# Kernel optimization log

Measured on AMD Instinct MI355X. Metric: run time of the kernel, lower is better.

## Reference

```python
import jax, jax.numpy as jnp
import numpy as np
from jax import lax

V, D_IN, H, B, T = 80, 8, 256, 4096, 80
W_SCALE = 1.0 / np.sqrt(H)  # matches torch nn.LSTM uniform init scale


def setup_inputs() -> dict:
    key = jax.random.key(0)
    ks = jax.random.split(key, 8)
    inp = {
        "x": jax.random.randint(ks[0], (B, T), 0, V),
        "h0": jnp.zeros((2, B, H), jnp.float32),
        "c0": jnp.zeros((2, B, H), jnp.float32),
        "emb": jax.random.normal(ks[1], (V, D_IN), jnp.float32),
        "W_ih0": jax.random.normal(ks[2], (4 * H, D_IN), jnp.float32) * W_SCALE,
        "W_hh0": jax.random.normal(ks[3], (4 * H, H), jnp.float32) * W_SCALE,
        "W_ih1": jax.random.normal(ks[4], (4 * H, H), jnp.float32) * W_SCALE,
        "W_hh1": jax.random.normal(ks[5], (4 * H, H), jnp.float32) * W_SCALE,
        "fc_W": jax.random.normal(ks[6], (V, H), jnp.float32) * W_SCALE,
        "fc_b": jnp.zeros((V,), jnp.float32),
    }
    return inp


def _lstm_layer(xs, h0, c0, W_ih, W_hh):
    # xs: [T, B, d_in]; precompute input contribution for all timesteps at once
    x_gates = jnp.einsum("tbd,gd->tbg", xs, W_ih)  # [T, B, 4H]

    def step(carry, xg):
        h, c = carry
        gates = xg + h @ W_hh.T  # [B, 4H], torch gate order i,f,g,o
        i, f, g, o = jnp.split(gates, 4, axis=-1)
        c = jax.nn.sigmoid(f) * c + jax.nn.sigmoid(i) * jnp.tanh(g)
        h = jax.nn.sigmoid(o) * jnp.tanh(c)
        return (h, c), h

    (hT, cT), hs = lax.scan(step, (h0, c0), x_gates)
    return hs, hT, cT  # hs: [T, B, H]


def reference(x, h0, c0, emb, W_ih0, W_hh0, W_ih1, W_hh1, fc_W, fc_b):
    xe = emb[x]                     # [B, T, D_IN] embedding lookup
    xs = jnp.swapaxes(xe, 0, 1)     # [T, B, D_IN] time-major for scan
    h1s, h1T, c1T = _lstm_layer(xs, h0[0], c0[0], W_ih0, W_hh0)
    h2s, h2T, c2T = _lstm_layer(h1s, h0[1], c0[1], W_ih1, W_hh1)
    logits = h2s[-1] @ fc_W.T + fc_b            # fc on last timestep: [B, V]
    h_n = jnp.stack([h1T, h2T])                  # [2, B, H]
    c_n = jnp.stack([c1T, c2T])
    return logits, h_n, c_n
```

## Files before the change

kernel.cpp:

```cpp
#include <hip/hip_runtime.h>
#include <hip/hip_bf16.h>
#include <stdint.h>

typedef __bf16 bf16x8 __attribute__((ext_vector_type(8)));
typedef float  f32x4  __attribute__((ext_vector_type(4)));

#define MFMA16(a, b, c) __builtin_amdgcn_mfma_f32_16x16x32_bf16((a), (b), (c), 0, 0, 0)

namespace {
constexpr int T_   = 80;
constexpr int B_   = 4096;
constexpr int H_   = 256;
constexpr int HP_  = 264;
constexpr int V_   = 80;
constexpr int RF   = 16;
constexpr int RC   = 32;
constexpr int NH   = 128;
constexpr int NTILE = 128;
constexpr int OUT_HN = B_ * V_;
constexpr int OUT_CN = OUT_HN + 2 * B_ * H_;

constexpr size_t WB_WHH0 = 0;
constexpr size_t WB_WIH1 = (size_t)1 << 20;
constexpr size_t WB_WHH1 = (size_t)2 << 20;
constexpr size_t WB_WIH0 = (size_t)3 << 20;
constexpr int WS_PLANE = 794624;
constexpr size_t WSB_XCHG  = 3178496;
constexpr size_t XCHG_U32  = (size_t)RC * NH;
constexpr size_t WSB_FLAGS = WSB_XCHG + (size_t)2 * 2 * NTILE * 2 * XCHG_U32 * 4;
constexpr int    CTRL_U32  = 512 + 256 + 8;
constexpr size_t WSB_TOTAL = WSB_FLAGS + (size_t)CTRL_U32 * 4;
}

__device__ __forceinline__ float sigm_(float x) { return 1.0f / (1.0f + __expf(-x)); }
__device__ __forceinline__ float tanh_(float x) {
  x = fminf(fmaxf(x, -15.f), 15.f);
  float e = __expf(2.f * x);
  return (e - 1.f) / (e + 1.f);
}

__device__ __forceinline__ void split_(float w, __hip_bfloat16* hi, __hip_bfloat16* lo) {
  __hip_bfloat16 h = __float2bfloat16(w);
  *hi = h;
  *lo = __float2bfloat16(w - __bfloat162float(h));
}

__device__ __forceinline__ uint32_t pack2_(__hip_bfloat16 hi, __hip_bfloat16 lo) {
  return (uint32_t)__builtin_bit_cast(unsigned short, hi) |
         ((uint32_t)__builtin_bit_cast(unsigned short, lo) << 16);
}
__device__ __forceinline__ __hip_bfloat16 ubf_(unsigned short v) {
  return __builtin_bit_cast(__hip_bfloat16, v);
}

__device__ __forceinline__ void ldfrag_(const char* pp, bf16x8* h, bf16x8* l) {
  *h = *(const bf16x8*)pp;
  *l = *(const bf16x8*)(pp + 16);
}

__device__ __forceinline__ size_t addrK256_(int e) {
  int row = e >> 8, kk = e & 255;
  int g = row >> 8, cb = row & 255, t = cb >> 4, m = cb & 15;
  int k = kk >> 5, quad = (kk >> 3) & 3, j = kk & 7;
  return (size_t)(((t * 8 + k) * 4 + g)) * 2048 + (size_t)((quad * 16 + m) * 32 + j * 2);
}

__global__ __launch_bounds__(256) void cvt_pair(
    const float* __restrict__ Wih0f, const float* __restrict__ Whh0f,
    const float* __restrict__ Wih1f, const float* __restrict__ Whh1f,
    __hip_bfloat16* __restrict__ ws, int zero_flags)
{
  if (zero_flags && blockIdx.x < 4) {
    uint32_t* fl = (uint32_t*)((char*)ws + WSB_FLAGS);
    int idx = blockIdx.x * 256 + threadIdx.x;
    if (idx < CTRL_U32) fl[idx] = 0u;
  }
  int i = blockIdx.x * 256 + threadIdx.x;
  if (i >= WS_PLANE) return;
  char* wb = (char*)ws;
  float v; size_t off;
  if (i < 262144) {
    v = Whh0f[i];            off = WB_WHH0 + addrK256_(i);
  } else if (i < 524288) {
    int e = i - 262144;
    v = Wih1f[e];            off = WB_WIH1 + addrK256_(e);
  } else if (i < 786432) {
    int e = i - 524288;
    v = Whh1f[e];            off = WB_WHH1 + addrK256_(e);
  } else {
    int e = i - 786432;
    int row = e >> 3, j = e & 7;
    int g = row >> 8, cb = row & 255, t = cb >> 4, m = cb & 15;
    v = Wih0f[e];
    off = WB_WIH0 + (size_t)((t * 4 + g) * 512 + m * 32 + j * 2);
  }
  __hip_bfloat16 hi = __float2bfloat16(v);
  *(__hip_bfloat16*)(wb + off)      = hi;
  *(__hip_bfloat16*)(wb + off + 16) = __float2bfloat16(v - __bfloat162float(hi));
}

__device__ __forceinline__ f32x4 tri_(bf16x8 ahi, bf16x8 alo, bf16x8 bhi, bf16x8 blo, f32x4 acc) {
  acc = MFMA16(ahi, bhi, acc);
  acc = MFMA16(ahi, blo, acc);
  acc = MFMA16(alo, bhi, acc);
  return acc;
}

__global__ __attribute__((amdgpu_waves_per_eu(2, 2))) __launch_bounds__(512)
void lstm_coop(
    const int* __restrict__ x,
    const float* __restrict__ h0,
    const float* __restrict__ c0,
    const float* __restrict__ emb,
    const __hip_bfloat16* __restrict__ wsW,
    const float* __restrict__ fcW,
    const float* __restrict__ fcb,
    float* __restrict__ out)
{
  __shared__ __align__(16) __hip_bfloat16 h1s[2][2][RC][HP_];
  __shared__ __align__(16) __hip_bfloat16 h2s[2][RC][HP_];
  __shared__ __align__(16) __hip_bfloat16 embs[2][V_][8];
  __shared__ unsigned short toks[RC][T_];
  __shared__ int slot_s;

  const int tid  = threadIdx.x;
  const int lane = tid & 63;
  const int wv   = tid >> 6;
  const int m    = lane & 15;
  const int quad = lane >> 4;
  const int jw   = wv * 16;
  const int lane32 = lane << 5;

  uint32_t* xch   = (uint32_t*)((char*)wsW + WSB_XCHG);
  uint32_t* flags = (uint32_t*)((char*)wsW + WSB_FLAGS);
  uint32_t* owner = flags + 512;
  uint32_t* cnt   = flags + 768;

  if (tid == 0) {
    uint32_t xcd;
    asm volatile("s_getreg_b32 %0, hwreg(20, 0, 4)" : "=s"(xcd));
    xcd &= 7u;
    uint32_t rank = atomicAdd(&cnt[xcd], 1u) & 31u;
    int p = (int)((xcd * 32u + rank) & 255u);
    while (atomicCAS(&owner[p], 0u, 1u) != 0u) p = (p + 1) & 255;
    slot_s = p;
  }
  __syncthreads();
  const int slot = slot_s;
  const int vx   = slot >> 5;
  const int rank = slot & 31;
  const int half = vx >> 2;
  const int tile = (vx & 3) * 32 + rank;
  const int r0   = tile * RC;
  const int oh   = half ^ 1;
  const int colb = half * NH + jw + m;
  const int tcol = half * 8 + wv;

  const char* wb    = (const char*)wsW;
  const char* pWhh0 = wb + WB_WHH0;
  const char* pWih1 = wb + WB_WIH1;
  const char* pWhh1 = wb + WB_WHH1;
  const char* pWih0 = wb + WB_WIH0;

  uint32_t* fl_own  = flags + half * NTILE + tile;
  uint32_t* fl_prt  = flags + oh   * NTILE + tile;
  uint32_t* fl_own1 = flags + 2 * NTILE + half * NTILE + tile;
  uint32_t* fl_prt1 = flags + 2 * NTILE + oh   * NTILE + tile;

  uint32_t* xo0 = xch + (((size_t)(0 * 2 + half) * NTILE + tile) * 2) * XCHG_U32;
  const uint32_t* xi0 = xch + (((size_t)(0 * 2 + oh) * NTILE + tile) * 2) * XCHG_U32;
  uint32_t* xo1 = xch + (((size_t)(1 * 2 + half) * NTILE + tile) * 2) * XCHG_U32;
  const uint32_t* xi1 = xch + (((size_t)(1 * 2 + oh) * NTILE + tile) * 2) * XCHG_U32;

  if (tid < V_) {
#pragma unroll
    for (int j = 0; j < 8; ++j)
      split_(emb[tid * 8 + j], &embs[0][tid][j], &embs[1][tid][j]);
  }
  for (int i = tid; i < RC * T_; i += 512) {
    int r = i / T_, tt = i - r * T_;
    int tok = x[(r0 + r) * T_ + tt];
    toks[r][tt] = (unsigned short)(tok < 0 ? 0 : (tok >= V_ ? V_ - 1 : tok));
  }
  for (int i = tid; i < RC * H_; i += 512) {
    int r = i >> 8, cc = i & 255;
    split_(h0[(0 * B_ + r0 + r) * H_ + cc], &h1s[1][0][r][cc], &h1s[1][1][r][cc]);
    split_(h0[(1 * B_ + r0 + r) * H_ + cc], &h2s[0][r][cc],    &h2s[1][r][cc]);
  }
  f32x4 c1[2], c2[2];
#pragma unroll
  for (int mt = 0; mt < 2; ++mt)
#pragma unroll
    for (int r = 0; r < 4; ++r) {
      int row = r0 + mt * 16 + quad * 4 + r;
      c1[mt][r] = c0[(0 * B_ + row) * H_ + colb];
      c2[mt][r] = c0[(1 * B_ + row) * H_ + colb];
    }

  bf16x8 zb;
#pragma unroll
  for (int j = 0; j < 8; ++j) zb[j] = (__bf16)0.0f;
  const f32x4 zf = {0.f, 0.f, 0.f, 0.f};

  __syncthreads();

  for (int t = 0; t < T_; ++t) {
    const int p = t & 1, q = p ^ 1;

    f32x4 acc[2][4];
    bf16x8 B0h[2][4], B0l[2][4];
#pragma unroll
    for (int g = 0; g < 4; ++g)
      ldfrag_(pWhh0 + ((size_t)((tcol * 8 + 0) * 4 + g) << 11) + lane32,
              &B0h[0][g], &B0l[0][g]);
    {
      bf16x8 eh0 = zb, el0 = zb, eh1 = zb, el1 = zb;
      if (quad == 0) {
        int t0 = toks[m][t], t1 = toks[16 + m][t];
        eh0 = *(const bf16x8*)&embs[0][t0][0]; el0 = *(const bf16x8*)&embs[1][t0][0];
        eh1 = *(const bf16x8*)&embs[0][t1][0]; el1 = *(const bf16x8*)&embs[1][t1][0];
      }
#pragma unroll
      for (int g = 0; g < 4; ++g) {
        bf16x8 Bh, Bl;
        ldfrag_(pWih0 + (size_t)((tcol * 4 + g) * 512 + (m << 5)), &Bh, &Bl);
        acc[0][g] = tri_(eh0, el0, Bh, Bl, zf);
        acc[1][g] = tri_(eh1, el1, Bh, Bl, zf);
      }
    }
#pragma unroll
    for (int k = 0; k < 8; ++k) {
      const int kb = k & 1, kn = kb ^ 1;
      if (k < 7) {
#pragma unroll
        for (int g = 0; g < 4; ++g)
          ldfrag_(pWhh0 + ((size_t)((tcol * 8 + k + 1) * 4 + g) << 11) + lane32,
                  &B0h[kn][g], &B0l[kn][g]);
      }
      const int ko = k * 32 + quad * 8;
      bf16x8 Ah0 = *(const bf16x8*)&h1s[q][0][m][ko];
      bf16x8 Al0 = *(const bf16x8*)&h1s[q][1][m][ko];
      bf16x8 Ah1 = *(const bf16x8*)&h1s[q][0][16 + m][ko];
      bf16x8 Al1 = *(const bf16x8*)&h1s[q][1][16 + m][ko];
#pragma unroll
      for (int g = 0; g < 4; ++g) {
        acc[0][g] = tri_(Ah0, Al0, B0h[kb][g], B0l[kb][g], acc[0][g]);
        acc[1][g] = tri_(Ah1, Al1, B0h[kb][g], B0l[kb][g], acc[1][g]);
      }
    }

    bf16x8 W1h[2][4], W1l[2][4];
#pragma unroll
    for (int g = 0; g < 4; ++g)
      ldfrag_(pWhh1 + ((size_t)((tcol * 8 + 0) * 4 + g) << 11) + lane32,
              &W1h[0][g], &W1l[0][g]);

    {
      uint32_t* xo = xo0 + (size_t)p * XCHG_U32;
#pragma unroll
      for (int mt = 0; mt < 2; ++mt)
#pragma unroll
        for (int r = 0; r < 4; ++r) {
          float ig = sigm_(acc[mt][0][r]);
          float fg = sigm_(acc[mt][1][r]);
          float gg = tanh_(acc[mt][2][r]);
          float og = sigm_(acc[mt][3][r]);
          float cn = fg * c1[mt][r] + ig * gg;
          c1[mt][r] = cn;
          float hv = og * tanh_(cn);
          int rr = mt * 16 + quad * 4 + r;
          __hip_bfloat16 hi, lo;
          split_(hv, &hi, &lo);
          h1s[p][0][rr][colb] = hi;
          h1s[p][1][rr][colb] = lo;
          __hip_atomic_store(&xo[rr * NH + jw + m], pack2_(hi, lo),
                             __ATOMIC_RELAXED, __HIP_MEMORY_SCOPE_AGENT);
        }
    }
    __syncthreads();
    if (tid == 0) {
      __hip_atomic_store(fl_own, (uint32_t)(t + 1),
                         __ATOMIC_RELAXED, __HIP_MEMORY_SCOPE_AGENT);
      while (__hip_atomic_load(fl_prt1, __ATOMIC_RELAXED,
                               __HIP_MEMORY_SCOPE_AGENT) < (uint32_t)t)
        __builtin_amdgcn_s_sleep(2);
    }
    __syncthreads();
    if (t > 0) {
      const uint64_t* xj = (const uint64_t*)(xi1 + (size_t)q * XCHG_U32);
      for (int i = tid; i < RC * NH / 2; i += 512) {
        uint64_t u = __hip_atomic_load(&xj[i], __ATOMIC_RELAXED, __HIP_MEMORY_SCOPE_AGENT);
        int row = i >> 6, c2 = (i & 63) * 2;
        uint32_t w0 = (uint32_t)u, w1 = (uint32_t)(u >> 32);
        h2s[0][row][oh * NH + c2]     = ubf_((unsigned short)(w0 & 0xffffu));
        h2s[1][row][oh * NH + c2]     = ubf_((unsigned short)(w0 >> 16));
        h2s[0][row][oh * NH + c2 + 1] = ubf_((unsigned short)(w1 & 0xffffu));
        h2s[1][row][oh * NH + c2 + 1] = ubf_((unsigned short)(w1 >> 16));
      }
    }
    __syncthreads();

#pragma unroll
    for (int mt = 0; mt < 2; ++mt)
#pragma unroll
      for (int g = 0; g < 4; ++g) acc[mt][g] = zf;
#pragma unroll
    for (int k = 0; k < 8; ++k) {
      const int kb = k & 1, kn = kb ^ 1;
      if (k < 7) {
#pragma unroll
        for (int g = 0; g < 4; ++g)
          ldfrag_(pWhh1 + ((size_t)((tcol * 8 + k + 1) * 4 + g) << 11) + lane32,
                  &W1h[kn][g], &W1l[kn][g]);
      }
      const int ko = k * 32 + quad * 8;
      bf16x8 Ch0 = *(const bf16x8*)&h2s[0][m][ko];
      bf16x8 Cl0 = *(const bf16x8*)&h2s[1][m][ko];
      bf16x8 Ch1 = *(const bf16x8*)&h2s[0][16 + m][ko];
      bf16x8 Cl1 = *(const bf16x8*)&h2s[1][16 + m][ko];
#pragma unroll
      for (int g = 0; g < 4; ++g) {
        acc[0][g] = tri_(Ch0, Cl0, W1h[kb][g], W1l[kb][g], acc[0][g]);
        acc[1][g] = tri_(Ch1, Cl1, W1h[kb][g], W1l[kb][g], acc[1][g]);
      }
    }

    bf16x8 W2h[2][4], W2l[2][4];
#pragma unroll
    for (int g = 0; g < 4; ++g)
      ldfrag_(pWih1 + ((size_t)((tcol * 8 + 0) * 4 + g) << 11) + lane32,
              &W2h[0][g], &W2l[0][g]);

    if (tid == 0) {
      while (__hip_atomic_load(fl_prt, __ATOMIC_RELAXED,
                               __HIP_MEMORY_SCOPE_AGENT) < (uint32_t)(t + 1))
        __builtin_amdgcn_s_sleep(2);
    }
    __syncthreads();
    {
      const uint64_t* xi = (const uint64_t*)(xi0 + (size_t)p * XCHG_U32);
      for (int i = tid; i < RC * NH / 2; i += 512) {
        uint64_t u = __hip_atomic_load(&xi[i], __ATOMIC_RELAXED, __HIP_MEMORY_SCOPE_AGENT);
        int row = i >> 6, c2 = (i & 63) * 2;
        uint32_t w0 = (uint32_t)u, w1 = (uint32_t)(u >> 32);
        h1s[p][0][row][oh * NH + c2]     = ubf_((unsigned short)(w0 & 0xffffu));
        h1s[p][1][row][oh * NH + c2]     = ubf_((unsigned short)(w0 >> 16));
        h1s[p][0][row][oh * NH + c2 + 1] = ubf_((unsigned short)(w1 & 0xffffu));
        h1s[p][1][row][oh * NH + c2 + 1] = ubf_((unsigned short)(w1 >> 16));
      }
    }
    __syncthreads();

#pragma unroll
    for (int k = 0; k < 8; ++k) {
      const int kb = k & 1, kn = kb ^ 1;
      if (k < 7) {
#pragma unroll
        for (int g = 0; g < 4; ++g)
          ldfrag_(pWih1 + ((size_t)((tcol * 8 + k + 1) * 4 + g) << 11) + lane32,
                  &W2h[kn][g], &W2l[kn][g]);
      }
      const int ko = k * 32 + quad * 8;
      bf16x8 Ah0 = *(const bf16x8*)&h1s[p][0][m][ko];
      bf16x8 Al0 = *(const bf16x8*)&h1s[p][1][m][ko];
      bf16x8 Ah1 = *(const bf16x8*)&h1s[p][0][16 + m][ko];
      bf16x8 Al1 = *(const bf16x8*)&h1s[p][1][16 + m][ko];
#pragma unroll
      for (int g = 0; g < 4; ++g) {
        acc[0][g] = tri_(Ah0, Al0, W2h[kb][g], W2l[kb][g], acc[0][g]);
        acc[1][g] = tri_(Ah1, Al1, W2h[kb][g], W2l[kb][g], acc[1][g]);
      }
    }

    {
      uint32_t* xo = xo1 + (size_t)p * XCHG_U32;
#pragma unroll
      for (int mt = 0; mt < 2; ++mt)
#pragma unroll
        for (int r = 0; r < 4; ++r) {
          float ig = sigm_(acc[mt][0][r]);
          float fg = sigm_(acc[mt][1][r]);
          float gg = tanh_(acc[mt][2][r]);
          float og = sigm_(acc[mt][3][r]);
          float cn = fg * c2[mt][r] + ig * gg;
          c2[mt][r] = cn;
          float hv = og * tanh_(cn);
          int rr = mt * 16 + quad * 4 + r;
          __hip_bfloat16 hi, lo;
          split_(hv, &hi, &lo);
          h2s[0][rr][colb] = hi;
          h2s[1][rr][colb] = lo;
          __hip_atomic_store(&xo[rr * NH + jw + m], pack2_(hi, lo),
                             __ATOMIC_RELAXED, __HIP_MEMORY_SCOPE_AGENT);
        }
    }
    __syncthreads();
    if (tid == 0)
      __hip_atomic_store(fl_own1, (uint32_t)(t + 1),
                         __ATOMIC_RELAXED, __HIP_MEMORY_SCOPE_AGENT);
  }

  if (tid == 0) {
    while (__hip_atomic_load(fl_prt1, __ATOMIC_RELAXED,
                             __HIP_MEMORY_SCOPE_AGENT) < (uint32_t)T_)
      __builtin_amdgcn_s_sleep(2);
  }
  __syncthreads();
  {
    const uint64_t* xj = (const uint64_t*)(xi1 + (size_t)((T_ - 1) & 1) * XCHG_U32);
    for (int i = tid; i < RC * NH / 2; i += 512) {
      uint64_t u = __hip_atomic_load(&xj[i], __ATOMIC_RELAXED, __HIP_MEMORY_SCOPE_AGENT);
      int row = i >> 6, c2 = (i & 63) * 2;
      uint32_t w0 = (uint32_t)u, w1 = (uint32_t)(u >> 32);
      h2s[0][row][oh * NH + c2]     = ubf_((unsigned short)(w0 & 0xffffu));
      h2s[1][row][oh * NH + c2]     = ubf_((unsigned short)(w0 >> 16));
      h2s[0][row][oh * NH + c2 + 1] = ubf_((unsigned short)(w1 & 0xffffu));
      h2s[1][row][oh * NH + c2 + 1] = ubf_((unsigned short)(w1 >> 16));
    }
  }
  __syncthreads();

  const int pf = (T_ - 1) & 1;

  for (int i = tid; i < RC * NH; i += 512) {
    int r = i >> 7, c = i & (NH - 1), col = half * NH + c;
    out[OUT_HN + (0 * B_ + r0 + r) * H_ + col] =
        __bfloat162float(h1s[pf][0][r][col]) + __bfloat162float(h1s[pf][1][r][col]);
    out[OUT_HN + (1 * B_ + r0 + r) * H_ + col] =
        __bfloat162float(h2s[0][r][col]) + __bfloat162float(h2s[1][r][col]);
  }
#pragma unroll
  for (int mt = 0; mt < 2; ++mt)
#pragma unroll
    for (int r = 0; r < 4; ++r) {
      int row = r0 + mt * 16 + quad * 4 + r;
      out[OUT_CN + row * H_ + colb]           = c1[mt][r];
      out[OUT_CN + B_ * H_ + row * H_ + colb] = c2[mt][r];
    }
  for (int i = tid; i < RC * (V_ / 2); i += 512) {
    int r = i / (V_ / 2), v = half * (V_ / 2) + i % (V_ / 2);
    const float* wp = fcW + v * H_;
    float s = fcb[v];
#pragma unroll 8
    for (int k = 0; k < H_; ++k) {
      float hk = __bfloat162float(h2s[0][r][k]) + __bfloat162float(h2s[1][r][k]);
      s += hk * wp[k];
    }
    out[(r0 + r) * V_ + v] = s;
  }
}

template<bool USE_WS>
__device__ __forceinline__ void loadB_(const char* wtb, int grp, int lane,
                                       const float* wf, int off,
                                       bf16x8* bhi, bf16x8* blo) {
  if (USE_WS) {
    const char* pp = wtb + ((size_t)grp << 11) + (lane << 5);
    *bhi = *(const bf16x8*)pp;
    *blo = *(const bf16x8*)(pp + 16);
  } else {
    f32x4 a = *(const f32x4*)(wf + off);
    f32x4 b = *(const f32x4*)(wf + off + 4);
#pragma unroll
    for (int j = 0; j < 4; ++j) {
      float w = a[j]; __bf16 h = (__bf16)w;
      (*bhi)[j] = h; (*blo)[j] = (__bf16)(w - (float)h);
    }
#pragma unroll
    for (int j = 0; j < 4; ++j) {
      float w = b[j]; __bf16 h = (__bf16)w;
      (*bhi)[4 + j] = h; (*blo)[4 + j] = (__bf16)(w - (float)h);
    }
  }
}

template<bool USE_WS>
__global__ __launch_bounds__(512, 2) void lstm_fused(
    const int* __restrict__ x,
    const float* __restrict__ h0,
    const float* __restrict__ c0,
    const float* __restrict__ emb,
    const __hip_bfloat16* __restrict__ wsW,
    const float* __restrict__ Wih0f,
    const float* __restrict__ Whh0f,
    const float* __restrict__ Wih1f,
    const float* __restrict__ Whh1f,
    const float* __restrict__ fcW,
    const float* __restrict__ fcb,
    float* __restrict__ out)
{
  __shared__ __align__(16) __hip_bfloat16 h1s[2][2][RF][HP_];
  __shared__ __align__(16) __hip_bfloat16 h2s[2][RF][HP_];
  __shared__ __align__(16) __hip_bfloat16 embs[2][V_][8];
  __shared__ __align__(16) __hip_bfloat16 es[2][RF][8];

  const int tid  = threadIdx.x;
  const int lane = tid & 63;
  const int wv   = tid >> 6;
  const int m    = lane & 15;
  const int quad = lane >> 4;
  const int jw   = wv * 32;
  const int r0   = blockIdx.x * RF;
  const char* wb = (const char*)wsW;

  if (tid < V_) {
#pragma unroll
    for (int j = 0; j < 8; ++j)
      split_(emb[tid * 8 + j], &embs[0][tid][j], &embs[1][tid][j]);
  }
  for (int i = tid; i < RF * H_; i += 512) {
    int r = i >> 8, cc = i & 255;
    split_(h0[(0 * B_ + r0 + r) * H_ + cc], &h1s[1][0][r][cc], &h1s[1][1][r][cc]);
    split_(h0[(1 * B_ + r0 + r) * H_ + cc], &h2s[0][r][cc],    &h2s[1][r][cc]);
  }
  f32x4 c1[2], c2[2];
#pragma unroll
  for (int ct = 0; ct < 2; ++ct)
#pragma unroll
    for (int r = 0; r < 4; ++r) {
      int row = r0 + quad * 4 + r;
      int col = jw + ct * 16 + m;
      c1[ct][r] = c0[(0 * B_ + row) * H_ + col];
      c2[ct][r] = c0[(1 * B_ + row) * H_ + col];
    }

  bf16x8 zb;
#pragma unroll
  for (int j = 0; j < 8; ++j) zb[j] = (__bf16)0.0f;
  const f32x4 zf = {0.f, 0.f, 0.f, 0.f};

  __syncthreads();

  for (int t = 0; t < T_; ++t) {
    const int p = t & 1, q = p ^ 1;

    if (tid < RF) {
      int tok = x[(r0 + tid) * T_ + t];
      tok = tok < 0 ? 0 : (tok >= V_ ? V_ - 1 : tok);
      *(bf16x8*)&es[0][tid][0] = *(const bf16x8*)&embs[0][tok][0];
      *(bf16x8*)&es[1][tid][0] = *(const bf16x8*)&embs[1][tok][0];
    }
    __syncthreads();

    f32x4 acc[8];
    {
      bf16x8 eh = zb, el = zb;
      if (quad == 0) {
        eh = *(const bf16x8*)&es[0][m][0];
        el = *(const bf16x8*)&es[1][m][0];
      }
#pragma unroll
      for (int g = 0; g < 4; ++g)
#pragma unroll
        for (int ct = 0; ct < 2; ++ct) {
          bf16x8 Bh = zb, Bl = zb;
          if (quad == 0) {
            if (USE_WS) {
              const char* pp = wb + WB_WIH0 +
                               (size_t)(((wv * 2 + ct) * 4 + g) * 512 + (m << 5));
              Bh = *(const bf16x8*)pp;
              Bl = *(const bf16x8*)(pp + 16);
            } else {
              const int off = (g * 256 + jw + ct * 16 + m) * 8;
              loadB_<false>(nullptr, 0, 0, Wih0f, off, &Bh, &Bl);
            }
          }
          acc[g * 2 + ct] = tri_(eh, el, Bh, Bl, zf);
        }
    }
#pragma unroll
    for (int k = 0; k < 8; ++k) {
      const int ko = k * 32 + quad * 8;
      bf16x8 Ah = *(const bf16x8*)&h1s[q][0][m][ko];
      bf16x8 Al = *(const bf16x8*)&h1s[q][1][m][ko];
#pragma unroll
      for (int g = 0; g < 4; ++g)
#pragma unroll
        for (int ct = 0; ct < 2; ++ct) {
          bf16x8 Bh, Bl;
          const int grp = ((wv * 2 + ct) * 8 + k) * 4 + g;
          const int off = (g * 256 + jw + ct * 16 + m) * H_ + ko;
          loadB_<USE_WS>(wb + WB_WHH0, grp, lane, Whh0f, off, &Bh, &Bl);
          acc[g * 2 + ct] = tri_(Ah, Al, Bh, Bl, acc[g * 2 + ct]);
        }
    }
#pragma unroll
    for (int ct = 0; ct < 2; ++ct)
#pragma unroll
      for (int r = 0; r < 4; ++r) {
        float ig = sigm_(acc[0 + ct][r]);
        float fg = sigm_(acc[2 + ct][r]);
        float gg = tanh_(acc[4 + ct][r]);
        float og = sigm_(acc[6 + ct][r]);
        float cn = fg * c1[ct][r] + ig * gg;
        c1[ct][r] = cn;
        float hv = og * tanh_(cn);
        int rr = quad * 4 + r, col = jw + ct * 16 + m;
        split_(hv, &h1s[p][0][rr][col], &h1s[p][1][rr][col]);
      }
    __syncthreads();

#pragma unroll
    for (int nt = 0; nt < 8; ++nt) acc[nt] = zf;
#pragma unroll
    for (int k = 0; k < 8; ++k) {
      const int ko = k * 32 + quad * 8;
      bf16x8 Ah = *(const bf16x8*)&h1s[p][0][m][ko];
      bf16x8 Al = *(const bf16x8*)&h1s[p][1][m][ko];
      bf16x8 Ch = *(const bf16x8*)&h2s[0][m][ko];
      bf16x8 Cl = *(const bf16x8*)&h2s[1][m][ko];
#pragma unroll
      for (int g = 0; g < 4; ++g)
#pragma unroll
        for (int ct = 0; ct < 2; ++ct) {
          const int grp = ((wv * 2 + ct) * 8 + k) * 4 + g;
          const int off = (g * 256 + jw + ct * 16 + m) * H_ + ko;
          bf16x8 Bh, Bl;
          loadB_<USE_WS>(wb + WB_WIH1, grp, lane, Wih1f, off, &Bh, &Bl);
          acc[g * 2 + ct] = tri_(Ah, Al, Bh, Bl, acc[g * 2 + ct]);
          loadB_<USE_WS>(wb + WB_WHH1, grp, lane, Whh1f, off, &Bh, &Bl);
          acc[g * 2 + ct] = tri_(Ch, Cl, Bh, Bl, acc[g * 2 + ct]);
        }
    }
    __syncthreads();

#pragma unroll
    for (int ct = 0; ct < 2; ++ct)
#pragma unroll
      for (int r = 0; r < 4; ++r) {
        float ig = sigm_(acc[0 + ct][r]);
        float fg = sigm_(acc[2 + ct][r]);
        float gg = tanh_(acc[4 + ct][r]);
        float og = sigm_(acc[6 + ct][r]);
        float cn = fg * c2[ct][r] + ig * gg;
        c2[ct][r] = cn;
        float hv = og * tanh_(cn);
        int rr = quad * 4 + r, col = jw + ct * 16 + m;
        split_(hv, &h2s[0][rr][col], &h2s[1][rr][col]);
      }
  }
  __syncthreads();

  const int pf = (T_ - 1) & 1;

  for (int i = tid; i < RF * H_; i += 512) {
    int r = i >> 8, cc = i & 255;
    out[OUT_HN + (0 * B_ + r0 + r) * H_ + cc] =
        __bfloat162float(h1s[pf][0][r][cc]) + __bfloat162float(h1s[pf][1][r][cc]);
    out[OUT_HN + (1 * B_ + r0 + r) * H_ + cc] =
        __bfloat162float(h2s[0][r][cc]) + __bfloat162float(h2s[1][r][cc]);
  }
#pragma unroll
  for (int ct = 0; ct < 2; ++ct)
#pragma unroll
    for (int r = 0; r < 4; ++r) {
      int row = r0 + quad * 4 + r;
      int col = jw + ct * 16 + m;
      out[OUT_CN + row * H_ + col]           = c1[ct][r];
      out[OUT_CN + B_ * H_ + row * H_ + col] = c2[ct][r];
    }
  for (int i = tid; i < RF * V_; i += 512) {
    int r = i / V_, v = i - r * V_;
    const float* wp = fcW + v * H_;
    float s = fcb[v];
#pragma unroll 8
    for (int k = 0; k < H_; ++k) {
      float hk = __bfloat162float(h2s[0][r][k]) + __bfloat162float(h2s[1][r][k]);
      s += hk * wp[k];
    }
    out[(r0 + r) * V_ + v] = s;
  }
}

extern "C" void kernel_launch(void* const* d_in, const int* in_sizes, int n_in,
                              void* d_out, int out_size, void* d_ws, size_t ws_size,
                              hipStream_t stream) {
  (void)in_sizes; (void)n_in; (void)out_size;
  const int*   x    = (const int*)d_in[0];
  const float* h0   = (const float*)d_in[1];
  const float* c0   = (const float*)d_in[2];
  const float* emb  = (const float*)d_in[3];
  const float* Wih0 = (const float*)d_in[4];
  const float* Whh0 = (const float*)d_in[5];
  const float* Wih1 = (const float*)d_in[6];
  const float* Whh1 = (const float*)d_in[7];
  const float* fcW  = (const float*)d_in[8];
  const float* fcb  = (const float*)d_in[9];
  float* outp = (float*)d_out;

  __hip_bfloat16* wsW = (__hip_bfloat16*)d_ws;

  if (ws_size >= WSB_TOTAL) {
    cvt_pair<<<(WS_PLANE + 255) / 256, 256, 0, stream>>>(Wih0, Whh0, Wih1, Whh1, wsW, 1);
    void* args[] = { (void*)&x, (void*)&h0, (void*)&c0, (void*)&emb, (void*)&wsW,
                     (void*)&fcW, (void*)&fcb, (void*)&outp };
    hipLaunchCooperativeKernel(reinterpret_cast<void*>(lstm_coop),
                               dim3(256), dim3(512), args, 0, stream);
  } else if (ws_size >= WSB_XCHG) {
    cvt_pair<<<(WS_PLANE + 255) / 256, 256, 0, stream>>>(Wih0, Whh0, Wih1, Whh1, wsW, 0);
    lstm_fused<true><<<B_ / RF, 512, 0, stream>>>(
        x, h0, c0, emb, wsW, Wih0, Whh0, Wih1, Whh1, fcW, fcb, outp);
  } else {
    lstm_fused<false><<<B_ / RF, 512, 0, stream>>>(
        x, h0, c0, emb, wsW, Wih0, Whh0, Wih1, Whh1, fcW, fcb, outp);
  }
}
```

Before: 3.064 ms.

## Split each tile's rows across two wave groups with 1024-thread blocks

Doubles the cooperative kernel's block to 1024 threads. Each group of 8 waves now handles 16 of the 32 rows per tile instead of each wave computing both 16-row M-tiles. This halves per-wave MFMA work and accumulator registers per timestep, putting more waves on the serial recurrence. The cost is that both row groups load the same weight fragments, which doubles weight traffic from global/L2 per block, and block-wide barriers now span more waves.

```diff
diff --git a/kernel.cpp b/kernel.cpp
--- a/kernel.cpp
+++ b/kernel.cpp
@@ -106,7 +106,7 @@
   return acc;
 }
 
-__global__ __attribute__((amdgpu_waves_per_eu(2, 2))) __launch_bounds__(512)
+__global__ __launch_bounds__(1024, 4)
 void lstm_coop(
     const int* __restrict__ x,
     const float* __restrict__ h0,
@@ -128,7 +128,10 @@
   const int wv   = tid >> 6;
   const int m    = lane & 15;
   const int quad = lane >> 4;
-  const int jw   = wv * 16;
+  const int ct   = wv & 7;
+  const int rh   = wv >> 3;
+  const int rbase = rh * 16;
+  const int jw   = ct * 16;
   const int lane32 = lane << 5;
 
   uint32_t* xch   = (uint32_t*)((char*)wsW + WSB_XCHG);
@@ -154,7 +157,7 @@
   const int r0   = tile * RC;
   const int oh   = half ^ 1;
   const int colb = half * NH + jw + m;
-  const int tcol = half * 8 + wv;
+  const int tcol = half * 8 + ct;
 
   const char* wb    = (const char*)wsW;
   const char* pWhh0 = wb + WB_WHH0;
@@ -177,25 +180,23 @@
     for (int j = 0; j < 8; ++j)
       split_(emb[tid * 8 + j], &embs[0][tid][j], &embs[1][tid][j]);
   }
-  for (int i = tid; i < RC * T_; i += 512) {
+  for (int i = tid; i < RC * T_; i += 1024) {
     int r = i / T_, tt = i - r * T_;
     int tok = x[(r0 + r) * T_ + tt];
     toks[r][tt] = (unsigned short)(tok < 0 ? 0 : (tok >= V_ ? V_ - 1 : tok));
   }
-  for (int i = tid; i < RC * H_; i += 512) {
+  for (int i = tid; i < RC * H_; i += 1024) {
     int r = i >> 8, cc = i & 255;
     split_(h0[(0 * B_ + r0 + r) * H_ + cc], &h1s[1][0][r][cc], &h1s[1][1][r][cc]);
     split_(h0[(1 * B_ + r0 + r) * H_ + cc], &h2s[0][r][cc],    &h2s[1][r][cc]);
   }
-  f32x4 c1[2], c2[2];
-#pragma unroll
-  for (int mt = 0; mt < 2; ++mt)
-#pragma unroll
-    for (int r = 0; r < 4; ++r) {
-      int row = r0 + mt * 16 + quad * 4 + r;
-      c1[mt][r] = c0[(0 * B_ + row) * H_ + colb];
-      c2[mt][r] = c0[(1 * B_ + row) * H_ + colb];
-    }
+  f32x4 c1, c2;
+#pragma unroll
+  for (int r = 0; r < 4; ++r) {
+    int row = r0 + rbase + quad * 4 + r;
+    c1[r] = c0[(0 * B_ + row) * H_ + colb];
+    c2[r] = c0[(1 * B_ + row) * H_ + colb];
+  }
 
   bf16x8 zb;
 #pragma unroll
@@ -207,25 +208,24 @@
   for (int t = 0; t < T_; ++t) {
     const int p = t & 1, q = p ^ 1;
 
-    f32x4 acc[2][4];
+    f32x4 acc[4];
     bf16x8 B0h[2][4], B0l[2][4];
 #pragma unroll
     for (int g = 0; g < 4; ++g)
       ldfrag_(pWhh0 + ((size_t)((tcol * 8 + 0) * 4 + g) << 11) + lane32,
               &B0h[0][g], &B0l[0][g]);
     {
-      bf16x8 eh0 = zb, el0 = zb, eh1 = zb, el1 = zb;
+      bf16x8 eh = zb, el = zb;
       if (quad == 0) {
-        int t0 = toks[m][t], t1 = toks[16 + m][t];
-        eh0 = *(const bf16x8*)&embs[0][t0][0]; el0 = *(const bf16x8*)&embs[1][t0][0];
-        eh1 = *(const bf16x8*)&embs[0][t1][0]; el1 = *(const bf16x8*)&embs[1][t1][0];
+        int t0 = toks[rbase + m][t];
+        eh = *(const bf16x8*)&embs[0][t0][0];
+        el = *(const bf16x8*)&embs[1][t0][0];
       }
 #pragma unroll
       for (int g = 0; g < 4; ++g) {
         bf16x8 Bh, Bl;
         ldfrag_(pWih0 + (size_t)((tcol * 4 + g) * 512 + (m << 5)), &Bh, &Bl);
-        acc[0][g] = tri_(eh0, el0, Bh, Bl, zf);
-        acc[1][g] = tri_(eh1, el1, Bh, Bl, zf);
+        acc[g] = tri_(eh, el, Bh, Bl, zf);
       }
     }
 #pragma unroll
@@ -238,15 +238,11 @@
                   &B0h[kn][g], &B0l[kn][g]);
       }
       const int ko = k * 32 + quad * 8;
-      bf16x8 Ah0 = *(const bf16x8*)&h1s[q][0][m][ko];
-      bf16x8 Al0 = *(const bf16x8*)&h1s[q][1][m][ko];
-      bf16x8 Ah1 = *(const bf16x8*)&h1s[q][0][16 + m][ko];
-      bf16x8 Al1 = *(const bf16x8*)&h1s[q][1][16 + m][ko];
-#pragma unroll
-      for (int g = 0; g < 4; ++g) {
-        acc[0][g] = tri_(Ah0, Al0, B0h[kb][g], B0l[kb][g], acc[0][g]);
-        acc[1][g] = tri_(Ah1, Al1, B0h[kb][g], B0l[kb][g], acc[1][g]);
-      }
+      bf16x8 Ah = *(const bf16x8*)&h1s[q][0][rbase + m][ko];
+      bf16x8 Al = *(const bf16x8*)&h1s[q][1][rbase + m][ko];
+#pragma unroll
+      for (int g = 0; g < 4; ++g)
+        acc[g] = tri_(Ah, Al, B0h[kb][g], B0l[kb][g], acc[g]);
     }
 
     bf16x8 W1h[2][4], W1l[2][4];
@@ -258,24 +254,22 @@
     {
       uint32_t* xo = xo0 + (size_t)p * XCHG_U32;
 #pragma unroll
-      for (int mt = 0; mt < 2; ++mt)
-#pragma unroll
-        for (int r = 0; r < 4; ++r) {
-          float ig = sigm_(acc[mt][0][r]);
-          float fg = sigm_(acc[mt][1][r]);
-          float gg = tanh_(acc[mt][2][r]);
-          float og = sigm_(acc[mt][3][r]);
-          float cn = fg * c1[mt][r] + ig * gg;
-          c1[mt][r] = cn;
-          float hv = og * tanh_(cn);
-          int rr = mt * 16 + quad * 4 + r;
-          __hip_bfloat16 hi, lo;
-          split_(hv, &hi, &lo);
-          h1s[p][0][rr][colb] = hi;
-          h1s[p][1][rr][colb] = lo;
-          __hip_atomic_store(&xo[rr * NH + jw + m], pack2_(hi, lo),
-                             __ATOMIC_RELAXED, __HIP_MEMORY_SCOPE_AGENT);
-        }
+      for (int r = 0; r < 4; ++r) {
+        float ig = sigm_(acc[0][r]);
+        float fg = sigm_(acc[1][r]);
+        float gg = tanh_(acc[2][r]);
+        float og = sigm_(acc[3][r]);
+        float cn = fg * c1[r] + ig * gg;
+        c1[r] = cn;
+        float hv = og * tanh_(cn);
+        int rr = rbase + quad * 4 + r;
+        __hip_bfloat16 hi, lo;
+        split_(hv, &hi, &lo);
+        h1s[p][0][rr][colb] = hi;
+        h1s[p][1][rr][colb] = lo;
+        __hip_atomic_store(&xo[rr * NH + jw + m], pack2_(hi, lo),
+                           __ATOMIC_RELAXED, __HIP_MEMORY_SCOPE_AGENT);
+      }
     }
     __syncthreads();
     if (tid == 0) {
@@ -288,22 +282,20 @@
     __syncthreads();
     if (t > 0) {
       const uint64_t* xj = (const uint64_t*)(xi1 + (size_t)q * XCHG_U32);
-      for (int i = tid; i < RC * NH / 2; i += 512) {
+      for (int i = tid; i < RC * NH / 2; i += 1024) {
         uint64_t u = __hip_atomic_load(&xj[i], __ATOMIC_RELAXED, __HIP_MEMORY_SCOPE_AGENT);
-        int row = i >> 6, c2 = (i & 63) * 2;
+        int row = i >> 6, c2v = (i & 63) * 2;
         uint32_t w0 = (uint32_t)u, w1 = (uint32_t)(u >> 32);
-        h2s[0][row][oh * NH + c2]     = ubf_((unsigned short)(w0 & 0xffffu));
-        h2s[1][row][oh * NH + c2]     = ubf_((unsigned short)(w0 >> 16));
-        h2s[0][row][oh * NH + c2 + 1] = ubf_((unsigned short)(w1 & 0xffffu));
-        h2s[1][row][oh * NH + c2 + 1] = ubf_((unsigned short)(w1 >> 16));
-      }
-    }
-    __syncthreads();
-
-#pragma unroll
-    for (int mt = 0; mt < 2; ++mt)
-#pragma unroll
-      for (int g = 0; g < 4; ++g) acc[mt][g] = zf;
+        h2s[0][row][oh * NH + c2v]     = ubf_((unsigned short)(w0 & 0xffffu));
+        h2s[1][row][oh * NH + c2v]     = ubf_((unsigned short)(w0 >> 16));
+        h2s[0][row][oh * NH + c2v + 1] = ubf_((unsigned short)(w1 & 0xffffu));
+        h2s[1][row][oh * NH + c2v + 1] = ubf_((unsigned short)(w1 >> 16));
+      }
+    }
+    __syncthreads();
+
+#pragma unroll
+    for (int g = 0; g < 4; ++g) acc[g] = zf;
 #pragma unroll
     for (int k = 0; k < 8; ++k) {
       const int kb = k & 1, kn = kb ^ 1;
@@ -314,15 +306,11 @@
                   &W1h[kn][g], &W1l[kn][g]);
       }
       const int ko = k * 32 + quad * 8;
-      bf16x8 Ch0 = *(const bf16x8*)&h2s[0][m][ko];
-      bf16x8 Cl0 = *(const bf16x8*)&h2s[1][m][ko];
-      bf16x8 Ch1 = *(const bf16x8*)&h2s[0][16 + m][ko];
-      bf16x8 Cl1 = *(const bf16x8*)&h2s[1][16 + m][ko];
-#pragma unroll
-      for (int g = 0; g < 4; ++g) {
-        acc[0][g] = tri_(Ch0, Cl0, W1h[kb][g], W1l[kb][g], acc[0][g]);
-        acc[1][g] = tri_(Ch1, Cl1, W1h[kb][g], W1l[kb][g], acc[1][g]);
-      }
+      bf16x8 Ch = *(const bf16x8*)&h2s[0][rbase + m][ko];
+      bf16x8 Cl = *(const bf16x8*)&h2s[1][rbase + m][ko];
+#pragma unroll
+      for (int g = 0; g < 4; ++g)
+        acc[g] = tri_(Ch, Cl, W1h[kb][g], W1l[kb][g], acc[g]);
     }
 
     bf16x8 W2h[2][4], W2l[2][4];
@@ -339,14 +327,14 @@
     __syncthreads();
     {
       const uint64_t* xi = (const uint64_t*)(xi0 + (size_t)p * XCHG_U32);
-      for (int i = tid; i < RC * NH / 2; i += 512) {
+      for (int i = tid; i < RC * NH / 2; i += 1024) {
         uint64_t u = __hip_atomic_load(&xi[i], __ATOMIC_RELAXED, __HIP_MEMORY_SCOPE_AGENT);
-        int row = i >> 6, c2 = (i & 63) * 2;
+        int row = i >> 6, c2v = (i & 63) * 2;
         uint32_t w0 = (uint32_t)u, w1 = (uint32_t)(u >> 32);
-        h1s[p][0][row][oh * NH + c2]     = ubf_((unsigned short)(w0 & 0xffffu));
-        h1s[p][1][row][oh * NH + c2]     = ubf_((unsigned short)(w0 >> 16));
-        h1s[p][0][row][oh * NH + c2 + 1] = ubf_((unsigned short)(w1 & 0xffffu));
-        h1s[p][1][row][oh * NH + c2 + 1] = ubf_((unsigned short)(w1 >> 16));
+        h1s[p][0][row][oh * NH + c2v]     = ubf_((unsigned short)(w0 & 0xffffu));
+        h1s[p][1][row][oh * NH + c2v]     = ubf_((unsigned short)(w0 >> 16));
+        h1s[p][0][row][oh * NH + c2v + 1] = ubf_((unsigned short)(w1 & 0xffffu));
+        h1s[p][1][row][oh * NH + c2v + 1] = ubf_((unsigned short)(w1 >> 16));
       }
     }
     __syncthreads();
@@ -361,38 +349,32 @@
                   &W2h[kn][g], &W2l[kn][g]);
       }
       const int ko = k * 32 + quad * 8;
-      bf16x8 Ah0 = *(const bf16x8*)&h1s[p][0][m][ko];
-      bf16x8 Al0 = *(const bf16x8*)&h1s[p][1][m][ko];
-      bf16x8 Ah1 = *(const bf16x8*)&h1s[p][0][16 + m][ko];
-      bf16x8 Al1 = *(const bf16x8*)&h1s[p][1][16 + m][ko];
-#pragma unroll
-      for (int g = 0; g < 4; ++g) {
-        acc[0][g] = tri_(Ah0, Al0, W2h[kb][g], W2l[kb][g], acc[0][g]);
-        acc[1][g] = tri_(Ah1, Al1, W2h[kb][g], W2l[kb][g], acc[1][g]);
-      }
+      bf16x8 Ah = *(const bf16x8*)&h1s[p][0][rbase + m][ko];
+      bf16x8 Al = *(const bf16x8*)&h1s[p][1][rbase + m][ko];
+#pragma unroll
+      for (int g = 0; g < 4; ++g)
+        acc[g] = tri_(Ah, Al, W2h[kb][g], W2l[kb][g], acc[g]);
     }
 
     {
       uint32_t* xo = xo1 + (size_t)p * XCHG_U32;
 #pragma unroll
-      for (int mt = 0; mt < 2; ++mt)
-#pragma unroll
-        for (int r = 0; r < 4; ++r) {
-          float ig = sigm_(acc[mt][0][r]);
-          float fg = sigm_(acc[mt][1][r]);
-          float gg = tanh_(acc[mt][2][r]);
-          float og = sigm_(acc[mt][3][r]);
-          float cn = fg * c2[mt][r] + ig * gg;
-          c2[mt][r] = cn;
-          float hv = og * tanh_(cn);
-          int rr = mt * 16 + quad * 4 + r;
-          __hip_bfloat16 hi, lo;
-          split_(hv, &hi, &lo);
-          h2s[0][rr][colb] = hi;
-          h2s[1][rr][colb] = lo;
-          __hip_atomic_store(&xo[rr * NH + jw + m], pack2_(hi, lo),
-                             __ATOMIC_RELAXED, __HIP_MEMORY_SCOPE_AGENT);
-        }
+      for (int r = 0; r < 4; ++r) {
+        float ig = sigm_(acc[0][r]);
+        float fg = sigm_(acc[1][r]);
+        float gg = tanh_(acc[2][r]);
+        float og = sigm_(acc[3][r]);
+        float cn = fg * c2[r] + ig * gg;
+        c2[r] = cn;
+        float hv = og * tanh_(cn);
+        int rr = rbase + quad * 4 + r;
+        __hip_bfloat16 hi, lo;
+        split_(hv, &hi, &lo);
+        h2s[0][rr][colb] = hi;
+        h2s[1][rr][colb] = lo;
+        __hip_atomic_store(&xo[rr * NH + jw + m], pack2_(hi, lo),
+                           __ATOMIC_RELAXED, __HIP_MEMORY_SCOPE_AGENT);
+      }
     }
     __syncthreads();
     if (tid == 0)
@@ -408,21 +390,21 @@
   __syncthreads();
   {
     const uint64_t* xj = (const uint64_t*)(xi1 + (size_t)((T_ - 1) & 1) * XCHG_U32);
-    for (int i = tid; i < RC * NH / 2; i += 512) {
+    for (int i = tid; i < RC * NH / 2; i += 1024) {
       uint64_t u = __hip_atomic_load(&xj[i], __ATOMIC_RELAXED, __HIP_MEMORY_SCOPE_AGENT);
-      int row = i >> 6, c2 = (i & 63) * 2;
+      int row = i >> 6, c2v = (i & 63) * 2;
       uint32_t w0 = (uint32_t)u, w1 = (uint32_t)(u >> 32);
-      h2s[0][row][oh * NH + c2]     = ubf_((unsigned short)(w0 & 0xffffu));
-      h2s[1][row][oh * NH + c2]     = ubf_((unsigned short)(w0 >> 16));
-      h2s[0][row][oh * NH + c2 + 1] = ubf_((unsigned short)(w1 & 0xffffu));
-      h2s[1][row][oh * NH + c2 + 1] = ubf_((unsigned short)(w1 >> 16));
+      h2s[0][row][oh * NH + c2v]     = ubf_((unsigned short)(w0 & 0xffffu));
+      h2s[1][row][oh * NH + c2v]     = ubf_((unsigned short)(w0 >> 16));
+      h2s[0][row][oh * NH + c2v + 1] = ubf_((unsigned short)(w1 & 0xffffu));
+      h2s[1][row][oh * NH + c2v + 1] = ubf_((unsigned short)(w1 >> 16));
     }
   }
   __syncthreads();
 
   const int pf = (T_ - 1) & 1;
 
-  for (int i = tid; i < RC * NH; i += 512) {
+  for (int i = tid; i < RC * NH; i += 1024) {
     int r = i >> 7, c = i & (NH - 1), col = half * NH + c;
     out[OUT_HN + (0 * B_ + r0 + r) * H_ + col] =
         __bfloat162float(h1s[pf][0][r][col]) + __bfloat162float(h1s[pf][1][r][col]);
@@ -430,14 +412,12 @@
         __bfloat162float(h2s[0][r][col]) + __bfloat162float(h2s[1][r][col]);
   }
 #pragma unroll
-  for (int mt = 0; mt < 2; ++mt)
-#pragma unroll
-    for (int r = 0; r < 4; ++r) {
-      int row = r0 + mt * 16 + quad * 4 + r;
-      out[OUT_CN + row * H_ + colb]           = c1[mt][r];
-      out[OUT_CN + B_ * H_ + row * H_ + colb] = c2[mt][r];
-    }
-  for (int i = tid; i < RC * (V_ / 2); i += 512) {
+  for (int r = 0; r < 4; ++r) {
+    int row = r0 + rbase + quad * 4 + r;
+    out[OUT_CN + row * H_ + colb]           = c1[r];
+    out[OUT_CN + B_ * H_ + row * H_ + colb] = c2[r];
+  }
+  for (int i = tid; i < RC * (V_ / 2); i += 1024) {
     int r = i / (V_ / 2), v = half * (V_ / 2) + i % (V_ / 2);
     const float* wp = fcW + v * H_;
     float s = fcb[v];
@@ -695,7 +675,7 @@
     void* args[] = { (void*)&x, (void*)&h0, (void*)&c0, (void*)&emb, (void*)&wsW,
                      (void*)&fcW, (void*)&fcb, (void*)&outp };
     hipLaunchCooperativeKernel(reinterpret_cast<void*>(lstm_coop),
-                               dim3(256), dim3(512), args, 0, stream);
+                               dim3(256), dim3(1024), args, 0, stream);
   } else if (ws_size >= WSB_XCHG) {
     cvt_pair<<<(WS_PLANE + 255) / 256, 256, 0, stream>>>(Wih0, Whh0, Wih1, Whh1, wsW, 0);
     lstm_fused<true><<<B_ / RF, 512, 0, stream>>>(
```

Measured after the change: 5.445 ms. +77.7%, slower.
